# Performance work log

Measured on AMD Instinct MI355X. Metric: run time of the kernel, lower is better.

Reference implementation:

```python
import jax, jax.numpy as jnp
import numpy as np

N_NODES = 100_000
N_EDGES = 1_600_000
N_GRAPHS = 512
HID = 64
NUM_CLASSES = 100
VOCAB = 3100
ID_OFFSET = 1500
BN_EPS = 1e-5


def setup_inputs() -> dict:
    key = jax.random.key(0)
    ks = jax.random.split(key, 8)
    node_ids = jax.random.randint(ks[0], (N_NODES,), 0, 1600)
    edge_src = jax.random.randint(ks[1], (N_EDGES,), 0, N_NODES)
    edge_dst = jax.random.randint(ks[2], (N_EDGES,), 0, N_NODES)
    graph_ids = jnp.sort(jax.random.randint(ks[3], (N_NODES,), 0, N_GRAPHS))
    emb = jax.random.normal(ks[4], (VOCAB, HID), dtype=jnp.float32) * 0.02
    # 3 GIN layers x 3 MLP linear layers, all 64->64 since embedding_dim == hidden
    Ws = jax.random.normal(ks[5], (3, 3, HID, HID), dtype=jnp.float32) * 0.05
    bs = jnp.zeros((3, 3, HID), dtype=jnp.float32)
    bn_gamma = jnp.ones((3, HID), dtype=jnp.float32)
    bn_beta = jnp.zeros((3, HID), dtype=jnp.float32)
    eps = jnp.zeros((3,), dtype=jnp.float32)  # learn_eps=True, init 0
    W_out = jax.random.normal(ks[6], (3 * HID, NUM_CLASSES), dtype=jnp.float32) * 0.05
    b_out = jnp.zeros((NUM_CLASSES,), dtype=jnp.float32)
    return {"node_ids": node_ids, "edge_src": edge_src, "edge_dst": edge_dst,
            "graph_ids": graph_ids, "emb": emb, "Ws": Ws, "bs": bs,
            "bn_gamma": bn_gamma, "bn_beta": bn_beta, "eps": eps,
            "W_out": W_out, "b_out": b_out}


def reference(node_ids, edge_src, edge_dst, graph_ids, emb, Ws, bs,
              bn_gamma, bn_beta, eps, W_out, b_out):
    n = node_ids.shape[0]
    h = emb[node_ids + ID_OFFSET]  # [N, HID]
    pooled = []
    for l in range(3):  # GIN layers (fixed small count)
        # GINConv, sum aggregator: (1+eps)*h + sum over in-edges of h[src]
        agg = jax.ops.segment_sum(h[edge_src], edge_dst, num_segments=n)
        x = (1.0 + eps[l]) * h + agg
        for m in range(3):
            x = jax.nn.relu(x @ Ws[l, m] + bs[l, m])
        mean = x.mean(axis=0)
        var = x.var(axis=0)  # biased var, as torch BN uses for normalization
        x = (x - mean) * jax.lax.rsqrt(var + BN_EPS) * bn_gamma[l] + bn_beta[l]
        h = x
        # dgl.sum_nodes: per-graph segment sum
        pooled.append(jax.ops.segment_sum(h, graph_ids, num_segments=N_GRAPHS))
    graph_features = jnp.concatenate(pooled, axis=-1)  # [G, 3*HID]
    return graph_features @ W_out + b_out  # [G, NUM_CLASSES]
```

## Files before the change

### kernel.cpp

```cpp
#include <hip/hip_runtime.h>

#define N_NODES 100000
#define N_EDGES 1600000
#define N_GRAPHS 512
#define HID 64
#define NUM_CLASSES 100
#define ID_OFFSET 1500
#define BN_EPS 1e-5f
#define CAP 64
#define NBKT 256
#define BSHIFT 9
#define NUSED ((N_NODES + 511) >> 9)
#define BCAP 10240
#define CBLK 98
#define CHUNK 16384
#define WPBLK 5
#define EMBBLK ((N_NODES * 32 + 1023) / 1024)
#define DUMMY_ROW 100000

typedef __attribute__((ext_vector_type(8))) short short8;
typedef __attribute__((ext_vector_type(4))) float floatx4;

__device__ __forceinline__ float b2f(unsigned short u) {
    return __builtin_bit_cast(float, ((unsigned)u) << 16);
}
__device__ __forceinline__ unsigned short f2b(float f) {
    unsigned x = __builtin_bit_cast(unsigned, f);
    x += 0x7FFFu + ((x >> 16) & 1u);
    return (unsigned short)(x >> 16);
}

#define XSH(row, qq) ((((((row) >> 4) << 7) + ((qq) << 4) + (((row) & 15) ^ (qq))) * 8))


__global__ __launch_bounds__(1024) void prep_kernel(const int* __restrict__ src,
                                                    const int* __restrict__ dst,
                                                    int* __restrict__ cursor,
                                                    int* __restrict__ rec,
                                                    const float* __restrict__ Ws,
                                                    unsigned short* __restrict__ whi,
                                                    unsigned short* __restrict__ wlo,
                                                    const int* __restrict__ node_ids,
                                                    const int* __restrict__ gid,
                                                    const float* __restrict__ emb,
                                                    unsigned short* __restrict__ h,
                                                    int* __restrict__ gs,
                                                    int* __restrict__ ge) {
    __shared__ int hist[NBKT];
    __shared__ int base_s[NBKT];
    int t = threadIdx.x;
    int blk = blockIdx.x;

    if (blk < CBLK) {
        if (t < NBKT) hist[t] = 0;
        __syncthreads();
        int cb = blk * CHUNK;
        int d_[16], s_[16];
#pragma unroll
        for (int k = 0; k < 16; ++k) {
            int i = cb + k * 1024 + t;
            d_[k] = (i < N_EDGES) ? dst[i] : -1;
            s_[k] = (i < N_EDGES) ? src[i] : 0;
            if (d_[k] >= 0) atomicAdd(&hist[((unsigned)d_[k] >> BSHIFT) & (NBKT - 1)], 1);
        }
        __syncthreads();
        if (t < NBKT) base_s[t] = (hist[t] > 0) ? atomicAdd(&cursor[t], hist[t]) : 0;
        __syncthreads();
        if (t < NBKT) hist[t] = 0;
        __syncthreads();
#pragma unroll
        for (int k = 0; k < 16; ++k) {
            if (d_[k] >= 0) {
                unsigned d = (unsigned)d_[k];
                int b = (d >> BSHIFT) & (NBKT - 1);
                int p = atomicAdd(&hist[b], 1);
                int g = base_s[b] + p;
                if ((unsigned)g < BCAP)
                    rec[b * BCAP + g] = ((int)(d & 511) << 17) | (s_[k] & 0x1FFFF);
            }
        }
    } else if (blk < CBLK + WPBLK) {
        int G = (blk - CBLK) * 1024 + t;
        if (G < 3 * 1536) {
            int l = G / 1536, Gp = G % 1536;
            int mm = Gp >> 9, rem = Gp & 511;
            int kq = rem >> 6, n = rem & 63;
            const float* Wp = Ws + l * 12288 + mm * 4096 + (kq * 8) * 64 + n;
            unsigned short uh[8], ul[8];
#pragma unroll
            for (int j = 0; j < 8; ++j) {
                float w = Wp[j * 64];
                unsigned short hi = f2b(w);
                uh[j] = hi;
                ul[j] = f2b(w - b2f(hi));
            }
            size_t off = (size_t)l * 12288 + (mm << 12) + XSH(n, kq);
            *(short8*)&whi[off] = *(short8*)uh;
            *(short8*)&wlo[off] = *(short8*)ul;
        }
    } else {
        int idx = (blk - CBLK - WPBLK) * 1024 + t;
        if (idx < N_NODES * 32) {
            int n = idx >> 5, cp = idx & 31;
            const float2 e = *(const float2*)(emb + (((size_t)(node_ids[n] + ID_OFFSET)) << 6) + cp * 2);
            unsigned v = (unsigned)f2b(e.x) | ((unsigned)f2b(e.y) << 16);
            ((unsigned*)h)[n * 32 + cp] = v;
            if (cp == 0) {
                int g = gid[n] & (N_GRAPHS - 1);
                if (n == 0 || (gid[n - 1] & (N_GRAPHS - 1)) != g) gs[g] = n;
                if (n == N_NODES - 1 || (gid[n + 1] & (N_GRAPHS - 1)) != g) ge[g] = n + 1;
            }
        }
    }
}


__global__ __launch_bounds__(1024) void fill_kernel(const int* __restrict__ rec,
                                                    const int* __restrict__ cursor,
                                                    int* __restrict__ cnt,
                                                    int* __restrict__ srcs) {
    __shared__ int lcnt[512];
    int t = threadIdx.x;
    int b = blockIdx.x;
    if (t < 512) lcnt[t] = 0;
    __syncthreads();
    int nb = cursor[b];
    if (nb < 0) nb = 0;
    if (nb > BCAP) nb = BCAP;
    const int* seg = rec + b * BCAP;
    for (int i = t; i < nb; i += 1024) {
        unsigned r = (unsigned)seg[i];
        int dl = (int)((r >> 17) & 511);
        int s = (int)(r & 0x1FFFF);
        int node = (b << BSHIFT) + dl;
        int p = atomicAdd(&lcnt[dl], 1);
        if (p < CAP && node < N_NODES) srcs[(node << 6) + p] = s;
    }
    __syncthreads();
    if (t < 512) {
        int node = (b << BSHIFT) + t;
        if (node < N_NODES) {
            int deg = lcnt[t];
            cnt[node] = deg;
            int degc = deg > CAP ? CAP : deg;
            int degp = (degc + 15) & ~15;
            if (degp < 16) degp = 16;
            for (int p = degc; p < degp; ++p) srcs[(node << 6) + p] = DUMMY_ROW;
        }
    }
}


__global__ __launch_bounds__(256) void agg_kernel(const unsigned short* __restrict__ x,
                                                  const int* __restrict__ cnt,
                                                  const int* __restrict__ srcs,
                                                  const float* __restrict__ eps, int l,
                                                  const float* __restrict__ stats,
                                                  const float* __restrict__ gamma,
                                                  const float* __restrict__ beta,
                                                  unsigned short* __restrict__ out) {
    int nb = __builtin_amdgcn_readfirstlane(((blockIdx.x << 2) + (threadIdx.x >> 6)) << 2);
    int lane = threadIdx.x & 63;
    int half = lane >> 5;
    int cl = lane & 31;
    const unsigned* __restrict__ xu = (const unsigned*)x;

    float scale = 1.0f + eps[l];
    float a0f = 1.0f, a1f = 1.0f, b0f = 0.0f, b1f = 0.0f;
    if (l > 0) {
        int lp = l - 1;
        float2 sm = *(const float2*)&stats[lp * 128 + 2 * cl];
        float2 sq = *(const float2*)&stats[lp * 128 + 64 + 2 * cl];
        float2 gm = *(const float2*)&gamma[lp * 64 + 2 * cl];
        float2 bt = *(const float2*)&beta[lp * 64 + 2 * cl];
        float mean0 = sm.x * (1.0f / N_NODES);
        float var0 = sq.x * (1.0f / N_NODES) - mean0 * mean0;
        float r0 = rsqrtf(var0 + BN_EPS);
        a0f = gm.x * r0;
        b0f = bt.x - mean0 * a0f;
        float mean1 = sm.y * (1.0f / N_NODES);
        float var1 = sq.y * (1.0f / N_NODES) - mean1 * mean1;
        float r1 = rsqrtf(var1 + BN_EPS);
        a1f = gm.y * r1;
        b1f = bt.y - mean1 * a1f;
    }

    int deg[4], degp[4];
    const int* row[4];
#pragma unroll
    for (int n = 0; n < 4; ++n) {
        int d = cnt[nb + n];
        int dc = d < 0 ? 0 : (d > CAP ? CAP : d);
        deg[n] = dc;
        int dp = (dc + 15) & ~15;
        degp[n] = dp < 16 ? 16 : dp;
        row[n] = srcs + ((size_t)(nb + n) << 6);
    }
    int cmax = degp[0];
    cmax = degp[1] > cmax ? degp[1] : cmax;
    cmax = degp[2] > cmax ? degp[2] : cmax;
    cmax = degp[3] > cmax ? degp[3] : cmax;

    unsigned us[4];
#pragma unroll
    for (int n = 0; n < 4; ++n) us[n] = xu[(size_t)(nb + n) * 32 + cl];

    float A0[4] = {0.f, 0.f, 0.f, 0.f}, A1[4] = {0.f, 0.f, 0.f, 0.f};
    float B0[4] = {0.f, 0.f, 0.f, 0.f}, B1[4] = {0.f, 0.f, 0.f, 0.f};

    {
        unsigned uv[4][8];
#pragma unroll
        for (int n = 0; n < 4; ++n)
#pragma unroll
            for (int k = 0; k < 8; ++k) {
                int ia = row[n][2 * k] & 0x1FFFF;
                int ib = row[n][2 * k + 1] & 0x1FFFF;
                int idx = half ? ib : ia;
                uv[n][k] = xu[(size_t)idx * 32 + cl];
            }
#pragma unroll
        for (int n = 0; n < 4; ++n)
#pragma unroll
            for (int k = 0; k < 8; ++k) {
                float lo = b2f((unsigned short)(uv[n][k] & 0xFFFF));
                float hi = b2f((unsigned short)(uv[n][k] >> 16));
                if (k & 1) { B0[n] += lo; B1[n] += hi; }
                else       { A0[n] += lo; A1[n] += hi; }
            }
    }

    for (int c = 16; c < cmax; c += 16) {
        unsigned uc[4][8];
#pragma unroll
        for (int n = 0; n < 4; ++n)
            if (c < degp[n])
#pragma unroll
                for (int k = 0; k < 8; ++k) {
                    int ia = row[n][c + 2 * k] & 0x1FFFF;
                    int ib = row[n][c + 2 * k + 1] & 0x1FFFF;
                    int idx = half ? ib : ia;
                    uc[n][k] = xu[(size_t)idx * 32 + cl];
                }
#pragma unroll
        for (int n = 0; n < 4; ++n)
            if (c < degp[n])
#pragma unroll
                for (int k = 0; k < 8; ++k) {
                    float lo = b2f((unsigned short)(uc[n][k] & 0xFFFF));
                    float hi = b2f((unsigned short)(uc[n][k] >> 16));
                    if (k & 1) { B0[n] += lo; B1[n] += hi; }
                    else       { A0[n] += lo; A1[n] += hi; }
                }
    }

#pragma unroll
    for (int n = 0; n < 4; ++n) {
        float S0 = (A0[n] + B0[n]);
        float S1 = (A1[n] + B1[n]);
        S0 += __shfl_xor(S0, 32);
        S1 += __shfl_xor(S1, 32);
        if (half == 0) {
            float selflo = b2f((unsigned short)(us[n] & 0xFFFF));
            float selfhi = b2f((unsigned short)(us[n] >> 16));
            float db = scale + (float)deg[n];
            float v0 = fmaf(a0f, fmaf(scale, selflo, S0), db * b0f);
            float v1 = fmaf(a1f, fmaf(scale, selfhi, S1), db * b1f);
            ((unsigned*)out)[(size_t)(nb + n) * 32 + cl] =
                (unsigned)f2b(v0) | ((unsigned)f2b(v1) << 16);
        }
    }
}


__global__ __launch_bounds__(256) void mlp_kernel(unsigned short* __restrict__ x,
                                                  const unsigned short* __restrict__ whi,
                                                  const unsigned short* __restrict__ wlo,
                                                  const float* __restrict__ bs, int l,
                                                  float* __restrict__ stats,
                                                  const int* __restrict__ graph_ids,
                                                  float* __restrict__ pooled, int last) {
    __shared__ __align__(16) unsigned short xs[128 * 64];
    __shared__ __align__(16) unsigned short wt[3 * 64 * 64];
    __shared__ int garr[128];
    __shared__ float ssum[256], sqq[256];
    int t = threadIdx.x;
    int nodebase = blockIdx.x * 128;
    int lane = t & 63, w = t >> 6;

    if (lane < 32) {
        int n = nodebase + w * 32 + lane;
        garr[w * 32 + lane] = (n < N_NODES) ? (graph_ids[n] & (N_GRAPHS - 1)) : -1;
    }
#pragma unroll
    for (int i = 0; i < 4; ++i) {
        int g = i * 64 + lane;
        int rl = g >> 3, qr = g & 7;
        int row = w * 32 + rl;
        const int4 v = *(const int4*)(x + (((size_t)(nodebase + row)) << 6) + qr * 8);
        *(int4*)&xs[XSH(row, qr)] = v;
    }
    {
        const unsigned short* wsrc = whi + (size_t)l * 12288;
#pragma unroll
        for (int i = 0; i < 6; ++i) {
            int g = i * 256 + t;
            *(int4*)&wt[g * 8] = *(const int4*)&wsrc[g * 8];
        }
    }
    __syncthreads();

    int m = lane & 15, q = lane >> 4;
    const float* bb = bs + l * 3 * 64;
    const unsigned short* wlol = wlo + (size_t)l * 12288;
    for (int mm = 0; mm < 3; ++mm) {
        short8 bl[2][4];
#pragma unroll
        for (int kc = 0; kc < 2; ++kc)
#pragma unroll
            for (int tj = 0; tj < 4; ++tj)
                bl[kc][tj] = *(const short8*)&wlol[(mm << 12) + XSH(tj * 16 + m, kc * 4 + q)];
        short8 a[2][2];
#pragma unroll
        for (int kc = 0; kc < 2; ++kc)
#pragma unroll
            for (int ti = 0; ti < 2; ++ti)
                a[kc][ti] = *(const short8*)&xs[XSH(w * 32 + ti * 16 + m, kc * 4 + q)];

        floatx4 acch[2][4], accl[2][4];
#pragma unroll
        for (int tj = 0; tj < 4; ++tj) {
            float bv = bb[mm * 64 + tj * 16 + m];
#pragma unroll
            for (int ti = 0; ti < 2; ++ti) {
                acch[ti][tj] = (floatx4){bv, bv, bv, bv};
                accl[ti][tj] = (floatx4){0.f, 0.f, 0.f, 0.f};
            }
        }
#pragma unroll
        for (int kc = 0; kc < 2; ++kc) {
            short8 bh[4];
#pragma unroll
            for (int tj = 0; tj < 4; ++tj)
                bh[tj] = *(const short8*)&wt[(mm << 12) + XSH(tj * 16 + m, kc * 4 + q)];
#pragma unroll
            for (int ti = 0; ti < 2; ++ti)
#pragma unroll
                for (int tj = 0; tj < 4; ++tj)
                    acch[ti][tj] = __builtin_amdgcn_mfma_f32_16x16x32_bf16(a[kc][ti], bh[tj], acch[ti][tj], 0, 0, 0);
        }
#pragma unroll
        for (int kc = 0; kc < 2; ++kc)
#pragma unroll
            for (int ti = 0; ti < 2; ++ti)
#pragma unroll
                for (int tj = 0; tj < 4; ++tj)
                    accl[ti][tj] = __builtin_amdgcn_mfma_f32_16x16x32_bf16(a[kc][ti], bl[kc][tj], accl[ti][tj], 0, 0, 0);
#pragma unroll
        for (int ti = 0; ti < 2; ++ti)
#pragma unroll
            for (int tj = 0; tj < 4; ++tj) {
                int col = tj * 16 + m;
#pragma unroll
                for (int r = 0; r < 4; ++r) {
                    int row = w * 32 + ti * 16 + q * 4 + r;
                    float v = acch[ti][tj][r] + accl[ti][tj][r];
                    xs[XSH(row, col >> 3) + (col & 7)] = f2b(v > 0.f ? v : 0.f);
                }
            }
    }

    if (!last) {
        unsigned* xo = (unsigned*)x;
#pragma unroll
        for (int it = 0; it < 16; ++it) {
            int row = w * 32 + (lane >> 5) + it * 2;
            int cp = lane & 31;
            int col = cp * 2;
            unsigned val = *(const unsigned*)&xs[XSH(row, col >> 3) + (col & 7)];
            int node = nodebase + row;
            if (node < N_NODES) xo[(size_t)node * 32 + cp] = val;
        }
    }
    {
        int c = lane;
        float s = 0.f, q2 = 0.f, acc2 = 0.f;
        int cur = -1;
        for (int k = 0; k < 32; ++k) {
            int row = w * 32 + k;
            int g = garr[row];
            if (g >= 0) {
                float v = b2f(xs[XSH(row, c >> 3) + (c & 7)]);
                s += v;
                q2 += v * v;
                if (g != cur) {
                    if (cur >= 0) atomicAdd(&pooled[cur * 192 + l * 64 + c], acc2);
                    acc2 = 0.f;
                    cur = g;
                }
                acc2 += v;
            }
        }
        if (cur >= 0) atomicAdd(&pooled[cur * 192 + l * 64 + c], acc2);
        ssum[t] = s;
        sqq[t] = q2;
    }
    __syncthreads();
    if (t < 64) {
        float S = ssum[t] + ssum[t + 64] + ssum[t + 128] + ssum[t + 192];
        float Q = sqq[t] + sqq[t + 64] + sqq[t + 128] + sqq[t + 192];
        atomicAdd(&stats[l * 128 + t], S);
        atomicAdd(&stats[l * 128 + 64 + t], Q);
    }
}


__global__ __launch_bounds__(256) void out_kernel(const float* __restrict__ pooled,
                                                  const float* __restrict__ stats,
                                                  const float* __restrict__ gamma,
                                                  const float* __restrict__ beta,
                                                  const int* __restrict__ gs,
                                                  const int* __restrict__ ge,
                                                  const float* __restrict__ Wo,
                                                  const float* __restrict__ bo,
                                                  float* __restrict__ out) {
    __shared__ float sab[384];
    int t = threadIdx.x;
    if (t < 192) {
        int l2 = t / 64, c = t & 63;
        float mean = stats[l2 * 128 + c] * (1.0f / N_NODES);
        float var = stats[l2 * 128 + 64 + c] * (1.0f / N_NODES) - mean * mean;
        float rstd = rsqrtf(var + BN_EPS);
        float a = gamma[l2 * 64 + c] * rstd;
        sab[l2 * 128 + c] = a;
        sab[l2 * 128 + 64 + c] = beta[l2 * 64 + c] - mean * a;
    }
    __syncthreads();
    int idx = blockIdx.x * blockDim.x + t;
    if (idx < N_GRAPHS * NUM_CLASSES) {
        int g = idx / NUM_CLASSES, k = idx % NUM_CLASSES;
        float cg = (float)(ge[g] - gs[g]);
        float acc = bo[k];
        for (int l2 = 0; l2 < 3; ++l2)
            for (int c = 0; c < 64; ++c) {
                float gf = fmaf(sab[l2 * 128 + c], pooled[g * 192 + l2 * 64 + c],
                                sab[l2 * 128 + 64 + c] * cg);
                acc = fmaf(gf, Wo[(l2 * 64 + c) * NUM_CLASSES + k], acc);
            }
        out[idx] = acc;
    }
}

extern "C" void kernel_launch(void* const* d_in, const int* in_sizes, int n_in,
                              void* d_out, int out_size, void* d_ws, size_t ws_size,
                              hipStream_t stream) {
    const int*   node_ids  = (const int*)d_in[0];
    const int*   edge_src  = (const int*)d_in[1];
    const int*   edge_dst  = (const int*)d_in[2];
    const int*   graph_ids = (const int*)d_in[3];
    const float* emb       = (const float*)d_in[4];
    const float* Ws        = (const float*)d_in[5];
    const float* bs        = (const float*)d_in[6];
    const float* gamma     = (const float*)d_in[7];
    const float* beta      = (const float*)d_in[8];
    const float* eps       = (const float*)d_in[9];
    const float* W_out     = (const float*)d_in[10];
    const float* b_out     = (const float*)d_in[11];
    float* out = (float*)d_out;

    unsigned short* h    = (unsigned short*)d_ws;
    unsigned short* xin  = h + 6400000 + 8192;
    unsigned short* whi  = xin + 6400000 + 8192;
    unsigned short* wlo  = whi + 36864;
    int*   srcs   = (int*)(wlo + 36864);
    int*   rec    = srcs + 6400000;
    float* pooled = (float*)(rec + NUSED * BCAP);
    float* stats  = pooled + 98304;
    int*   cnt    = (int*)(stats + 384);
    int*   gs     = cnt + 100000;
    int*   ge     = gs + 512;
    int*   cursor = ge + 512;

    hipMemsetAsync(pooled, 0,
                   (size_t)(98304 + 384 + 100000 + 512 + 512 + 256) * 4, stream);
    hipMemsetAsync(h + (size_t)DUMMY_ROW * 64, 0, 128, stream);
    hipMemsetAsync(xin + (size_t)DUMMY_ROW * 64, 0, 128, stream);

    prep_kernel<<<CBLK + WPBLK + EMBBLK, 1024, 0, stream>>>(
        edge_src, edge_dst, cursor, rec, Ws, whi, wlo,
        node_ids, graph_ids, emb, h, gs, ge);
    fill_kernel<<<NUSED, 1024, 0, stream>>>(rec, cursor, cnt, srcs);

    const int MLP_BLK = (N_NODES + 127) / 128;
    const int AGG_BLK = N_NODES / 16;
    for (int l = 0; l < 3; ++l) {
        unsigned short* X = (l % 2 == 0) ? h : xin;
        unsigned short* A = (l % 2 == 0) ? xin : h;
        agg_kernel<<<AGG_BLK, 256, 0, stream>>>(X, cnt, srcs, eps, l, stats, gamma, beta, A);
        mlp_kernel<<<MLP_BLK, 256, 0, stream>>>(A, whi, wlo, bs, l, stats, graph_ids, pooled, l == 2);
    }

    out_kernel<<<(N_GRAPHS * NUM_CLASSES + 255) / 256, 256, 0, stream>>>(
        pooled, stats, gamma, beta, gs, ge, W_out, b_out, out);
}
```

Measured before the change: 336.7 us.

## Fuse neighbor aggregation into MLP kernel, keeping aggregated rows in LDS

Merges agg_kernel and mlp_kernel into a single per-layer kernel. Each wave gathers and sums neighbor rows for its 32 nodes, eight at a time, and writes the result straight into the shared-memory tile that the MFMA MLP reads. This removes the global write and re-read of the aggregated features and one launch per layer. In exchange it uses more registers (8-node batches) and has fewer waves in flight for the latency-bound gather, since each block now holds a large LDS footprint.

```diff
diff --git a/kernel.cpp b/kernel.cpp
--- a/kernel.cpp
+++ b/kernel.cpp
@@ -151,19 +151,41 @@
 }
 
 
-__global__ __launch_bounds__(256) void agg_kernel(const unsigned short* __restrict__ x,
-                                                  const int* __restrict__ cnt,
-                                                  const int* __restrict__ srcs,
-                                                  const float* __restrict__ eps, int l,
-                                                  const float* __restrict__ stats,
-                                                  const float* __restrict__ gamma,
-                                                  const float* __restrict__ beta,
-                                                  unsigned short* __restrict__ out) {
-    int nb = __builtin_amdgcn_readfirstlane(((blockIdx.x << 2) + (threadIdx.x >> 6)) << 2);
-    int lane = threadIdx.x & 63;
-    int half = lane >> 5;
-    int cl = lane & 31;
+__global__ __launch_bounds__(256) void fused_kernel(const unsigned short* __restrict__ x,
+                                                    unsigned short* __restrict__ xo,
+                                                    const int* __restrict__ cnt,
+                                                    const int* __restrict__ srcs,
+                                                    const float* __restrict__ eps, int l,
+                                                    float* __restrict__ stats,
+                                                    const float* __restrict__ gamma,
+                                                    const float* __restrict__ beta,
+                                                    const unsigned short* __restrict__ whi,
+                                                    const unsigned short* __restrict__ wlo,
+                                                    const float* __restrict__ bs,
+                                                    const int* __restrict__ graph_ids,
+                                                    float* __restrict__ pooled, int last) {
+    __shared__ __align__(16) unsigned short xs[128 * 64];
+    __shared__ __align__(16) unsigned short wt[3 * 64 * 64];
+    __shared__ int garr[128];
+    __shared__ float ssum[256], sqq[256];
+    int t = threadIdx.x;
+    int nodebase = blockIdx.x * 128;
+    int lane = t & 63, w = t >> 6;
+    int half = lane >> 5, cl = lane & 31;
     const unsigned* __restrict__ xu = (const unsigned*)x;
+
+    if (lane < 32) {
+        int n = nodebase + w * 32 + lane;
+        garr[w * 32 + lane] = (n < N_NODES) ? (graph_ids[n] & (N_GRAPHS - 1)) : -1;
+    }
+    {
+        const unsigned short* wsrc = whi + (size_t)l * 12288;
+#pragma unroll
+        for (int i = 0; i < 6; ++i) {
+            int g = i * 256 + t;
+            *(int4*)&wt[g * 8] = *(const int4*)&wsrc[g * 8];
+        }
+    }
 
     float scale = 1.0f + eps[l];
     float a0f = 1.0f, a1f = 1.0f, b0f = 0.0f, b1f = 0.0f;
@@ -185,127 +207,95 @@
         b1f = bt.y - mean1 * a1f;
     }
 
-    int deg[4], degp[4];
-    const int* row[4];
-#pragma unroll
-    for (int n = 0; n < 4; ++n) {
-        int d = cnt[nb + n];
-        int dc = d < 0 ? 0 : (d > CAP ? CAP : d);
-        deg[n] = dc;
-        int dp = (dc + 15) & ~15;
-        degp[n] = dp < 16 ? 16 : dp;
-        row[n] = srcs + ((size_t)(nb + n) << 6);
-    }
-    int cmax = degp[0];
-    cmax = degp[1] > cmax ? degp[1] : cmax;
-    cmax = degp[2] > cmax ? degp[2] : cmax;
-    cmax = degp[3] > cmax ? degp[3] : cmax;
-
-    unsigned us[4];
-#pragma unroll
-    for (int n = 0; n < 4; ++n) us[n] = xu[(size_t)(nb + n) * 32 + cl];
-
-    float A0[4] = {0.f, 0.f, 0.f, 0.f}, A1[4] = {0.f, 0.f, 0.f, 0.f};
-    float B0[4] = {0.f, 0.f, 0.f, 0.f}, B1[4] = {0.f, 0.f, 0.f, 0.f};
-
-    {
-        unsigned uv[4][8];
-#pragma unroll
-        for (int n = 0; n < 4; ++n)
-#pragma unroll
-            for (int k = 0; k < 8; ++k) {
-                int ia = row[n][2 * k] & 0x1FFFF;
-                int ib = row[n][2 * k + 1] & 0x1FFFF;
-                int idx = half ? ib : ia;
-                uv[n][k] = xu[(size_t)idx * 32 + cl];
-            }
-#pragma unroll
-        for (int n = 0; n < 4; ++n)
-#pragma unroll
-            for (int k = 0; k < 8; ++k) {
-                float lo = b2f((unsigned short)(uv[n][k] & 0xFFFF));
-                float hi = b2f((unsigned short)(uv[n][k] >> 16));
-                if (k & 1) { B0[n] += lo; B1[n] += hi; }
-                else       { A0[n] += lo; A1[n] += hi; }
-            }
-    }
-
-    for (int c = 16; c < cmax; c += 16) {
-        unsigned uc[4][8];
-#pragma unroll
-        for (int n = 0; n < 4; ++n)
-            if (c < degp[n])
+    int wb = __builtin_amdgcn_readfirstlane(nodebase + w * 32);
+
+    for (int g8 = 0; g8 < 4; ++g8) {
+        int nb = wb + g8 * 8;
+        int deg[8], degp[8];
+        const int* row[8];
+#pragma unroll
+        for (int n = 0; n < 8; ++n) {
+            int d = cnt[nb + n];
+            int dc = d < 0 ? 0 : (d > CAP ? CAP : d);
+            deg[n] = dc;
+            int dp = (dc + 15) & ~15;
+            degp[n] = dp < 16 ? 16 : dp;
+            row[n] = srcs + ((size_t)(nb + n) << 6);
+        }
+        int cmax = degp[0];
+#pragma unroll
+        for (int n = 1; n < 8; ++n) cmax = degp[n] > cmax ? degp[n] : cmax;
+
+        unsigned us[8];
+#pragma unroll
+        for (int n = 0; n < 8; ++n) us[n] = xu[(size_t)(nb + n) * 32 + cl];
+
+        float A0[8], A1[8], B0[8], B1[8];
+#pragma unroll
+        for (int n = 0; n < 8; ++n) { A0[n] = 0.f; A1[n] = 0.f; B0[n] = 0.f; B1[n] = 0.f; }
+
+        {
+            unsigned uv[8][8];
+#pragma unroll
+            for (int n = 0; n < 8; ++n)
 #pragma unroll
                 for (int k = 0; k < 8; ++k) {
-                    int ia = row[n][c + 2 * k] & 0x1FFFF;
-                    int ib = row[n][c + 2 * k + 1] & 0x1FFFF;
+                    int ia = row[n][2 * k] & 0x1FFFF;
+                    int ib = row[n][2 * k + 1] & 0x1FFFF;
                     int idx = half ? ib : ia;
-                    uc[n][k] = xu[(size_t)idx * 32 + cl];
+                    uv[n][k] = xu[(size_t)idx * 32 + cl];
                 }
 #pragma unroll
-        for (int n = 0; n < 4; ++n)
-            if (c < degp[n])
+            for (int n = 0; n < 8; ++n)
 #pragma unroll
                 for (int k = 0; k < 8; ++k) {
-                    float lo = b2f((unsigned short)(uc[n][k] & 0xFFFF));
-                    float hi = b2f((unsigned short)(uc[n][k] >> 16));
+                    float lo = b2f((unsigned short)(uv[n][k] & 0xFFFF));
+                    float hi = b2f((unsigned short)(uv[n][k] >> 16));
                     if (k & 1) { B0[n] += lo; B1[n] += hi; }
                     else       { A0[n] += lo; A1[n] += hi; }
                 }
-    }
-
-#pragma unroll
-    for (int n = 0; n < 4; ++n) {
-        float S0 = (A0[n] + B0[n]);
-        float S1 = (A1[n] + B1[n]);
-        S0 += __shfl_xor(S0, 32);
-        S1 += __shfl_xor(S1, 32);
-        if (half == 0) {
-            float selflo = b2f((unsigned short)(us[n] & 0xFFFF));
-            float selfhi = b2f((unsigned short)(us[n] >> 16));
-            float db = scale + (float)deg[n];
-            float v0 = fmaf(a0f, fmaf(scale, selflo, S0), db * b0f);
-            float v1 = fmaf(a1f, fmaf(scale, selfhi, S1), db * b1f);
-            ((unsigned*)out)[(size_t)(nb + n) * 32 + cl] =
-                (unsigned)f2b(v0) | ((unsigned)f2b(v1) << 16);
-        }
-    }
-}
-
-
-__global__ __launch_bounds__(256) void mlp_kernel(unsigned short* __restrict__ x,
-                                                  const unsigned short* __restrict__ whi,
-                                                  const unsigned short* __restrict__ wlo,
-                                                  const float* __restrict__ bs, int l,
-                                                  float* __restrict__ stats,
-                                                  const int* __restrict__ graph_ids,
-                                                  float* __restrict__ pooled, int last) {
-    __shared__ __align__(16) unsigned short xs[128 * 64];
-    __shared__ __align__(16) unsigned short wt[3 * 64 * 64];
-    __shared__ int garr[128];
-    __shared__ float ssum[256], sqq[256];
-    int t = threadIdx.x;
-    int nodebase = blockIdx.x * 128;
-    int lane = t & 63, w = t >> 6;
-
-    if (lane < 32) {
-        int n = nodebase + w * 32 + lane;
-        garr[w * 32 + lane] = (n < N_NODES) ? (graph_ids[n] & (N_GRAPHS - 1)) : -1;
-    }
-#pragma unroll
-    for (int i = 0; i < 4; ++i) {
-        int g = i * 64 + lane;
-        int rl = g >> 3, qr = g & 7;
-        int row = w * 32 + rl;
-        const int4 v = *(const int4*)(x + (((size_t)(nodebase + row)) << 6) + qr * 8);
-        *(int4*)&xs[XSH(row, qr)] = v;
-    }
-    {
-        const unsigned short* wsrc = whi + (size_t)l * 12288;
-#pragma unroll
-        for (int i = 0; i < 6; ++i) {
-            int g = i * 256 + t;
-            *(int4*)&wt[g * 8] = *(const int4*)&wsrc[g * 8];
+        }
+        for (int c = 16; c < cmax; c += 16) {
+            unsigned uc[8][8];
+#pragma unroll
+            for (int n = 0; n < 8; ++n)
+                if (c < degp[n])
+#pragma unroll
+                    for (int k = 0; k < 8; ++k) {
+                        int ia = row[n][c + 2 * k] & 0x1FFFF;
+                        int ib = row[n][c + 2 * k + 1] & 0x1FFFF;
+                        int idx = half ? ib : ia;
+                        uc[n][k] = xu[(size_t)idx * 32 + cl];
+                    }
+#pragma unroll
+            for (int n = 0; n < 8; ++n)
+                if (c < degp[n])
+#pragma unroll
+                    for (int k = 0; k < 8; ++k) {
+                        float lo = b2f((unsigned short)(uc[n][k] & 0xFFFF));
+                        float hi = b2f((unsigned short)(uc[n][k] >> 16));
+                        if (k & 1) { B0[n] += lo; B1[n] += hi; }
+                        else       { A0[n] += lo; A1[n] += hi; }
+                    }
+        }
+
+#pragma unroll
+        for (int n = 0; n < 8; ++n) {
+            float S0 = A0[n] + B0[n];
+            float S1 = A1[n] + B1[n];
+            S0 += __shfl_xor(S0, 32);
+            S1 += __shfl_xor(S1, 32);
+            if (half == 0) {
+                float selflo = b2f((unsigned short)(us[n] & 0xFFFF));
+                float selfhi = b2f((unsigned short)(us[n] >> 16));
+                float db = scale + (float)deg[n];
+                float v0 = fmaf(a0f, fmaf(scale, selflo, S0), db * b0f);
+                float v1 = fmaf(a1f, fmaf(scale, selfhi, S1), db * b1f);
+                int r = w * 32 + g8 * 8 + n;
+                int col = 2 * cl;
+                *(unsigned*)&xs[XSH(r, col >> 3) + (col & 7)] =
+                    (unsigned)f2b(v0) | ((unsigned)f2b(v1) << 16);
+            }
         }
     }
     __syncthreads();
@@ -371,7 +361,7 @@
     }
 
     if (!last) {
-        unsigned* xo = (unsigned*)x;
+        unsigned* xou = (unsigned*)xo;
 #pragma unroll
         for (int it = 0; it < 16; ++it) {
             int row = w * 32 + (lane >> 5) + it * 2;
@@ -379,7 +369,7 @@
             int col = cp * 2;
             unsigned val = *(const unsigned*)&xs[XSH(row, col >> 3) + (col & 7)];
             int node = nodebase + row;
-            if (node < N_NODES) xo[(size_t)node * 32 + cp] = val;
+            if (node < N_NODES) xou[(size_t)node * 32 + cp] = val;
         }
     }
     {
@@ -491,13 +481,13 @@
         node_ids, graph_ids, emb, h, gs, ge);
     fill_kernel<<<NUSED, 1024, 0, stream>>>(rec, cursor, cnt, srcs);
 
-    const int MLP_BLK = (N_NODES + 127) / 128;
-    const int AGG_BLK = N_NODES / 16;
+    const int FUSE_BLK = (N_NODES + 127) / 128;
     for (int l = 0; l < 3; ++l) {
-        unsigned short* X = (l % 2 == 0) ? h : xin;
+        const unsigned short* X = (l % 2 == 0) ? h : xin;
         unsigned short* A = (l % 2 == 0) ? xin : h;
-        agg_kernel<<<AGG_BLK, 256, 0, stream>>>(X, cnt, srcs, eps, l, stats, gamma, beta, A);
-        mlp_kernel<<<MLP_BLK, 256, 0, stream>>>(A, whi, wlo, bs, l, stats, graph_ids, pooled, l == 2);
+        fused_kernel<<<FUSE_BLK, 256, 0, stream>>>(
+            X, A, cnt, srcs, eps, l, stats, gamma, beta,
+            whi, wlo, bs, graph_ids, pooled, l == 2);
     }
 
     out_kernel<<<(N_GRAPHS * NUM_CLASSES + 255) / 256, 256, 0, stream>>>(
```

Result: slower. 658.5 us (+95.6%).
